# Optimization experiments

Hardware: AMD Instinct MI355X
Metric: run time of the kernel (lower is better)

## Reference

```python
import jax, jax.numpy as jnp
import numpy as np

B, T, D, H = 64, 512, 1024, 2048


def setup_inputs() -> dict:
    key = jax.random.key(0)
    ks = jax.random.split(key, 7)
    s_ih = 1.0 / np.sqrt(H)
    return {
        "x": jax.random.normal(ks[0], (B, T, D), dtype=jnp.float32),
        "W_ih": jax.random.normal(ks[1], (4 * H, D), dtype=jnp.float32) * s_ih,
        "W_hh": jax.random.normal(ks[2], (4 * H, H), dtype=jnp.float32) * s_ih,
        "b_ih": jax.random.normal(ks[3], (4 * H,), dtype=jnp.float32) * s_ih,
        "b_hh": jax.random.normal(ks[4], (4 * H,), dtype=jnp.float32) * s_ih,
        "W_head": jax.random.normal(ks[5], (D, H), dtype=jnp.float32) * (1.0 / np.sqrt(H)),
        "b_head": jax.random.normal(ks[6], (D,), dtype=jnp.float32) * 0.01,
    }


def reference(x, W_ih, W_hh, b_ih, b_hh, W_head, b_head):
    Bn, Tn, Dn = x.shape
    Hn = W_hh.shape[1]
    # precompute input projections for all timesteps: [T, B, 4H]
    x_proj = jnp.einsum('btd,gd->tbg', x, W_ih) + (b_ih + b_hh)

    def step(carry, xp_t):
        h, c = carry
        gates = xp_t + h @ W_hh.T  # [B, 4H]
        i, f, g, o = jnp.split(gates, 4, axis=-1)  # PyTorch gate order: i,f,g,o
        i = jax.nn.sigmoid(i)
        f = jax.nn.sigmoid(f)
        g = jnp.tanh(g)
        o = jax.nn.sigmoid(o)
        c = f * c + i * g
        h = o * jnp.tanh(c)
        return (h, c), None

    h0 = jnp.zeros((Bn, Hn), dtype=x.dtype)
    c0 = jnp.zeros((Bn, Hn), dtype=x.dtype)
    (h, c), _ = jax.lax.scan(step, (h0, c0), x_proj)
    return h @ W_head.T + b_head  # [B, D]
```

## Files before the change

kernel.cpp:

```cpp
#include <hip/hip_runtime.h>
#include <hip/hip_bf16.h>
#include <cstdint>
#include <cstddef>

#define BB 64
#define TT 512
#define DD 1024
#define HH 2048
#define GG 8192

typedef unsigned short u16;
typedef __attribute__((ext_vector_type(8))) short bf16x8;
typedef __attribute__((ext_vector_type(4))) float f32x4;

__device__ __forceinline__ u16 f2bf(float f) {
  union { float f; uint32_t u; } v; v.f = f;
  uint32_t r = v.u + 0x7FFFu + ((v.u >> 16) & 1u);
  return (u16)(r >> 16);
}
__device__ __forceinline__ float bf2f(u16 h) {
  union { uint32_t u; float f; } v; v.u = ((uint32_t)h) << 16; return v.f;
}

__device__ __forceinline__ bf16x8 cvt8(const float* __restrict__ p) {
  float4 a = *(const float4*)p;
  float4 b = *(const float4*)(p + 4);
  bf16x8 r;
  r[0] = (short)f2bf(a.x); r[1] = (short)f2bf(a.y);
  r[2] = (short)f2bf(a.z); r[3] = (short)f2bf(a.w);
  r[4] = (short)f2bf(b.x); r[5] = (short)f2bf(b.y);
  r[6] = (short)f2bf(b.z); r[7] = (short)f2bf(b.w);
  return r;
}

__device__ __forceinline__ bf16x8 cohload16(const u16* p) {
  bf16x8 v;
  asm volatile("global_load_dwordx4 %0, %1, off sc0 sc1" : "=v"(v) : "v"(p));
  return v;
}
__device__ __forceinline__ void cohstore16(u16* p, bf16x8 v) {
  asm volatile("global_store_dwordx4 %0, %1, off sc0 sc1" :: "v"(p), "v"(v) : "memory");
}

__global__ void conv_wih_kernel(const float* __restrict__ W, u16* __restrict__ Wb) {
  size_t idx = (size_t)blockIdx.x * blockDim.x + threadIdx.x;
  if (idx >= (size_t)GG * DD / 8) return;
  *(bf16x8*)(Wb + idx * 8) = cvt8(W + idx * 8);
}

__global__ void conv_xT_kernel(const float* __restrict__ x, u16* __restrict__ xbT) {
  size_t idx = (size_t)blockIdx.x * blockDim.x + threadIdx.x;
  if (idx >= (size_t)BB * TT * DD / 8) return;
  const int col8 = (int)(idx & 127);
  const int row = (int)(idx >> 7);
  const int b = row >> 9, t = row & 511;
  bf16x8 v = cvt8(x + (size_t)row * DD + col8 * 8);
  *(bf16x8*)(xbT + ((size_t)t * BB + b) * DD + col8 * 8) = v;
}

template<int XMODE>
__global__ __launch_bounds__(512, 1)
void lstm_persistent(const float* __restrict__ x, const u16* __restrict__ xbT,
                     const u16* __restrict__ wihb, const float* __restrict__ W_hh,
                     const float* __restrict__ b_ih, const float* __restrict__ b_hh,
                     u16* __restrict__ h0, u16* __restrict__ h1,
                     int* __restrict__ arrv, int* __restrict__ gof) {
  __shared__ u16 Wlds[64 * 2 * 64 * 8];
  __shared__ float red[4 * 2 * 64 * 4];
  __shared__ float gst[64 * 36];
  __shared__ u16 hsh[512];

  const int tid = threadIdx.x;
  const int wave = tid >> 6, lane = tid & 63;
  const int m = wave & 3, khalf = wave >> 2;
  const int c = lane & 15, g = lane >> 4;
  const int wg = blockIdx.x, j0 = wg * 8;

  {
    const int r = tid >> 4;
    const int gr = (r < 8) ? (j0 + r) : (r < 16) ? (HH + j0 + r - 8)
                 : (r < 24) ? (2 * HH + j0 + r - 16) : (3 * HH + j0 + r - 24);
    const int which = r >> 4, cc = r & 15;
    const float* src = W_hh + (size_t)gr * HH;
    const int k0 = (tid & 15) * 128;
    #pragma unroll
    for (int k8 = 0; k8 < 16; ++k8) {
      const int k = k0 + k8 * 8;
      bf16x8 v = cvt8(src + k);
      const int ent = ((k >> 5) * 2 + which) * 64 + ((k >> 3) & 3) * 16 + cc;
      *(bf16x8*)(Wlds + (size_t)ent * 8) = v;
    }
  }

  const int tb = tid >> 3, tj = tid & 7;
  const int jg = j0 + tj;
  const float bia = b_ih[jg] + b_hh[jg];
  const float bfa = b_ih[HH + jg] + b_hh[HH + jg];
  const float bga = b_ih[2 * HH + jg] + b_hh[2 * HH + jg];
  const float boa = b_ih[3 * HH + jg] + b_hh[3 * HH + jg];
  float cst = 0.f;

  const int arow = m * 16 + c;
  const int r0 = (c < 8) ? (j0 + c) : (HH + j0 + c - 8);
  const int r1 = (c < 8) ? (2 * HH + j0 + c) : (3 * HH + j0 + c - 8);

  __syncthreads();

  for (int t = 0; t < TT; ++t) {
    const u16* hs = (t & 1) ? h1 : h0;
    u16* hd = (t & 1) ? h0 : h1;
    f32x4 acc0 = {0.f, 0.f, 0.f, 0.f};
    f32x4 acc1 = {0.f, 0.f, 0.f, 0.f};

    #pragma unroll 4
    for (int i = 0; i < 16; ++i) {
      const int k = khalf * 512 + i * 32 + g * 8;
      bf16x8 a;
      if constexpr (XMODE == 1) a = *(const bf16x8*)(xbT + ((size_t)t * BB + arow) * DD + k);
      else                      a = cvt8(x + ((size_t)arow * TT + t) * DD + k);
      bf16x8 b0 = *(const bf16x8*)(wihb + (size_t)r0 * DD + k);
      bf16x8 b1 = *(const bf16x8*)(wihb + (size_t)r1 * DD + k);
      acc0 = __builtin_amdgcn_mfma_f32_16x16x32_bf16(a, b0, acc0, 0, 0, 0);
      acc1 = __builtin_amdgcn_mfma_f32_16x16x32_bf16(a, b1, acc1, 0, 0, 0);
    }

    if (t > 0) {
      if (wg == 0) {
        if (tid < 256) {
          int iters = 0;
          while (__hip_atomic_load(arrv + tid * 16, __ATOMIC_RELAXED, __HIP_MEMORY_SCOPE_AGENT) < t) {
            __builtin_amdgcn_s_sleep(1);
            if (++iters > (1 << 17)) break;
          }
        }
        __syncthreads();
        if (tid < 256)
          __hip_atomic_store(gof + tid * 16, t, __ATOMIC_RELAXED, __HIP_MEMORY_SCOPE_AGENT);
      } else {
        if (tid == 0) {
          int iters = 0;
          while (__hip_atomic_load(gof + wg * 16, __ATOMIC_RELAXED, __HIP_MEMORY_SCOPE_AGENT) < t) {
            __builtin_amdgcn_s_sleep(1);
            if (++iters > (1 << 17)) break;
          }
        }
      }
    }
    __syncthreads();

    {
      bf16x8 hf[32];
      const u16* hrow = hs + (size_t)arow * HH + g * 8;
      #pragma unroll
      for (int i = 0; i < 32; ++i)
        hf[i] = cohload16(hrow + (size_t)(khalf * 32 + i) * 32);

      #pragma unroll
      for (int grp = 0; grp < 4; ++grp) {
        if (grp == 0)      asm volatile("s_waitcnt vmcnt(24)" ::: "memory");
        else if (grp == 1) asm volatile("s_waitcnt vmcnt(16)" ::: "memory");
        else if (grp == 2) asm volatile("s_waitcnt vmcnt(8)"  ::: "memory");
        else               asm volatile("s_waitcnt vmcnt(0)"  ::: "memory");
        __builtin_amdgcn_sched_barrier(0);
        #pragma unroll
        for (int i2 = 0; i2 < 8; ++i2) {
          const int i = grp * 8 + i2;
          const int kb = khalf * 32 + i;
          bf16x8 b0 = *(const bf16x8*)(Wlds + (size_t)((kb * 2 + 0) * 64 + lane) * 8);
          bf16x8 b1 = *(const bf16x8*)(Wlds + (size_t)((kb * 2 + 1) * 64 + lane) * 8);
          acc0 = __builtin_amdgcn_mfma_f32_16x16x32_bf16(hf[i], b0, acc0, 0, 0, 0);
          acc1 = __builtin_amdgcn_mfma_f32_16x16x32_bf16(hf[i], b1, acc1, 0, 0, 0);
        }
      }
    }

    if (khalf == 1) {
      #pragma unroll
      for (int q = 0; q < 4; ++q) {
        red[((m * 2 + 0) * 64 + lane) * 4 + q] = acc0[q];
        red[((m * 2 + 1) * 64 + lane) * 4 + q] = acc1[q];
      }
    }
    __syncthreads();
    if (khalf == 0) {
      #pragma unroll
      for (int q = 0; q < 4; ++q) {
        const float s0 = acc0[q] + red[((m * 2 + 0) * 64 + lane) * 4 + q];
        const float s1 = acc1[q] + red[((m * 2 + 1) * 64 + lane) * 4 + q];
        const int b = m * 16 + g * 4 + q;
        gst[b * 36 + c] = s0;
        gst[b * 36 + 16 + c] = s1;
      }
    }
    __syncthreads();

    {
      const float ip = gst[tb * 36 + tj]      + bia;
      const float fp = gst[tb * 36 + 8 + tj]  + bfa;
      const float gp = gst[tb * 36 + 16 + tj] + bga;
      const float op = gst[tb * 36 + 24 + tj] + boa;
      const float ig = 1.f / (1.f + expf(-ip));
      const float fg = 1.f / (1.f + expf(-fp));
      const float gv = tanhf(gp);
      const float og = 1.f / (1.f + expf(-op));
      cst = fg * cst + ig * gv;
      hsh[tb * 8 + tj] = f2bf(og * tanhf(cst));
    }
    __syncthreads();

    if (tid < 64) {
      bf16x8 v = *(const bf16x8*)(hsh + tid * 8);
      cohstore16(hd + (size_t)tid * HH + j0, v);
      asm volatile("s_waitcnt vmcnt(0)" ::: "memory");
    }
    __syncthreads();
    if (tid == 0)
      __hip_atomic_store(arrv + wg * 16, t + 1, __ATOMIC_RELAXED, __HIP_MEMORY_SCOPE_AGENT);
  }
}

__global__ __launch_bounds__(512)
void lstm_step_kernel(const float* __restrict__ x,
                      const float* __restrict__ W_ih, const float* __restrict__ W_hh,
                      const float* __restrict__ b_ih, const float* __restrict__ b_hh,
                      const u16* __restrict__ h_src, u16* __restrict__ h_dst,
                      float* __restrict__ cbuf, int t) {
  const int tid = threadIdx.x;
  const int wave = tid >> 6, lane = tid & 63;
  const int m = wave & 3, khalf = wave >> 2;
  const int j0 = blockIdx.x * 8;
  const int c = lane & 15;
  const int arow = m * 16 + c;
  const int koff = (lane >> 4) * 8;
  const int r0 = (c < 8) ? (j0 + c) : (HH + j0 + c - 8);
  const int r1 = (c < 8) ? (2 * HH + j0 + c) : (3 * HH + j0 + c - 8);

  f32x4 acc0 = {0.f, 0.f, 0.f, 0.f};
  f32x4 acc1 = {0.f, 0.f, 0.f, 0.f};

  if (khalf == 0) {
    const size_t xrow = ((size_t)arow * TT + t) * DD;
    #pragma unroll 4
    for (int kb = 0; kb < 32; ++kb) {
      const int k = kb * 32 + koff;
      bf16x8 a = cvt8(x + xrow + k);
      bf16x8 b0 = cvt8(W_ih + (size_t)r0 * DD + k);
      bf16x8 b1 = cvt8(W_ih + (size_t)r1 * DD + k);
      acc0 = __builtin_amdgcn_mfma_f32_16x16x32_bf16(a, b0, acc0, 0, 0, 0);
      acc1 = __builtin_amdgcn_mfma_f32_16x16x32_bf16(a, b1, acc1, 0, 0, 0);
    }
    #pragma unroll 4
    for (int kb = 0; kb < 16; ++kb) {
      const int kh = kb * 32 + koff;
      bf16x8 a = *(const bf16x8*)(h_src + (size_t)arow * HH + kh);
      bf16x8 b0 = cvt8(W_hh + (size_t)r0 * HH + kh);
      bf16x8 b1 = cvt8(W_hh + (size_t)r1 * HH + kh);
      acc0 = __builtin_amdgcn_mfma_f32_16x16x32_bf16(a, b0, acc0, 0, 0, 0);
      acc1 = __builtin_amdgcn_mfma_f32_16x16x32_bf16(a, b1, acc1, 0, 0, 0);
    }
  } else {
    #pragma unroll 4
    for (int kb = 0; kb < 48; ++kb) {
      const int kh = 512 + kb * 32 + koff;
      bf16x8 a = *(const bf16x8*)(h_src + (size_t)arow * HH + kh);
      bf16x8 b0 = cvt8(W_hh + (size_t)r0 * HH + kh);
      bf16x8 b1 = cvt8(W_hh + (size_t)r1 * HH + kh);
      acc0 = __builtin_amdgcn_mfma_f32_16x16x32_bf16(a, b0, acc0, 0, 0, 0);
      acc1 = __builtin_amdgcn_mfma_f32_16x16x32_bf16(a, b1, acc1, 0, 0, 0);
    }
  }

  __shared__ float red[4][2][64][4];
  if (khalf == 1) {
    #pragma unroll
    for (int q = 0; q < 4; ++q) { red[m][0][lane][q] = acc0[q]; red[m][1][lane][q] = acc1[q]; }
  }
  __syncthreads();
  if (khalf == 1) return;
  #pragma unroll
  for (int q = 0; q < 4; ++q) { acc0[q] += red[m][0][lane][q]; acc1[q] += red[m][1][lane][q]; }

  const float bias0 = b_ih[r0] + b_hh[r0];
  const float bias1 = b_ih[r1] + b_hh[r1];
  #pragma unroll
  for (int q = 0; q < 4; ++q) { acc0[q] += bias0; acc1[q] += bias1; }

  float fpre[4], opre[4];
  #pragma unroll
  for (int q = 0; q < 4; ++q) {
    fpre[q] = __shfl_xor(acc0[q], 8);
    opre[q] = __shfl_xor(acc1[q], 8);
  }

  if (c < 8) {
    const int j = j0 + c;
    #pragma unroll
    for (int q = 0; q < 4; ++q) {
      const int b = m * 16 + (lane >> 4) * 4 + q;
      const float ig = 1.f / (1.f + expf(-acc0[q]));
      const float fg = 1.f / (1.f + expf(-fpre[q]));
      const float gg = tanhf(acc1[q]);
      const float og = 1.f / (1.f + expf(-opre[q]));
      const float cold = cbuf[(size_t)b * HH + j];
      const float cn = fg * cold + ig * gg;
      cbuf[(size_t)b * HH + j] = cn;
      h_dst[(size_t)b * HH + j] = f2bf(og * tanhf(cn));
    }
  }
}

__global__ __launch_bounds__(256)
void head_kernel(const u16* __restrict__ hfin, const float* __restrict__ W_head,
                 const float* __restrict__ b_head, float* __restrict__ out) {
  const int tid = threadIdx.x, wave = tid >> 6, lane = tid & 63;
  const int m = wave;
  const int c = lane & 15;
  const int koff = (lane >> 4) * 8;
  const int d = blockIdx.x * 16 + c;
  const int arow = m * 16 + c;
  f32x4 acc = {0.f, 0.f, 0.f, 0.f};
  #pragma unroll 4
  for (int kb = 0; kb < 64; ++kb) {
    const int k = kb * 32 + koff;
    bf16x8 a = *(const bf16x8*)(hfin + (size_t)arow * HH + k);
    bf16x8 b = cvt8(W_head + (size_t)d * HH + k);
    acc = __builtin_amdgcn_mfma_f32_16x16x32_bf16(a, b, acc, 0, 0, 0);
  }
  const float bh = b_head[d];
  #pragma unroll
  for (int q = 0; q < 4; ++q) {
    const int b = m * 16 + (lane >> 4) * 4 + q;
    out[(size_t)b * DD + d] = acc[q] + bh;
  }
}

extern "C" void kernel_launch(void* const* d_in, const int* in_sizes, int n_in,
                              void* d_out, int out_size, void* d_ws, size_t ws_size,
                              hipStream_t stream) {
  const float* x      = (const float*)d_in[0];
  const float* W_ih   = (const float*)d_in[1];
  const float* W_hh   = (const float*)d_in[2];
  const float* b_ih   = (const float*)d_in[3];
  const float* b_hh   = (const float*)d_in[4];
  const float* W_head = (const float*)d_in[5];
  const float* b_head = (const float*)d_in[6];
  float* out = (float*)d_out;

  char* ws = (char*)d_ws;
  u16*  h0    = (u16*)(ws + 0);
  u16*  h1    = (u16*)(ws + 256 * 1024);
  int*  arrv  = (int*)(ws + 512 * 1024);
  int*  gof   = (int*)(ws + 544 * 1024);
  float* cbuf = (float*)(ws + 512 * 1024);
  u16*  wihb  = (u16*)(ws + (1ull << 20));
  u16*  xbT   = (u16*)(ws + (17ull << 20));

  const size_t NEED1 = (81ull << 20);
  const size_t NEED0 = (17ull << 20);

  hipMemsetAsync(ws, 0, 1u << 20, stream);

  if (ws_size >= NEED0) {
    {
      const int n8 = (int)((size_t)GG * DD / 8);
      conv_wih_kernel<<<(n8 + 255) / 256, 256, 0, stream>>>(W_ih, wihb);
    }
    if (ws_size >= NEED1) {
      const int n8 = (int)((size_t)BB * TT * DD / 8);
      conv_xT_kernel<<<(n8 + 255) / 256, 256, 0, stream>>>(x, xbT);
      lstm_persistent<1><<<256, 512, 0, stream>>>(x, xbT, wihb, W_hh, b_ih, b_hh, h0, h1, arrv, gof);
    } else {
      lstm_persistent<0><<<256, 512, 0, stream>>>(x, xbT, wihb, W_hh, b_ih, b_hh, h0, h1, arrv, gof);
    }
  } else {
    for (int t = 0; t < TT; ++t) {
      u16* hs = (t & 1) ? h1 : h0;
      u16* hd = (t & 1) ? h0 : h1;
      lstm_step_kernel<<<256, 512, 0, stream>>>(x, W_ih, W_hh, b_ih, b_hh, hs, hd, cbuf, t);
    }
  }

  head_kernel<<<64, 256, 0, stream>>>(h0, W_head, b_head, out);
}
```

Measured before the change: 10.46 ms.

## Stage hidden state per XCD into L2 before recurrent matmul loads

Each workgroup finds its XCD and takes a rank within it. At every timestep the 32 workgroups on that XCD copy the full hidden state from the coherent buffer into a per-XCD staging buffer and meet at a per-XCD counter barrier. The recurrent matmul then reads h with L2-cacheable loads instead of loads that bypass the cache to memory. This is meant to cut the latency and memory traffic of 256 workgroups all reading h uncached. The cost is an extra copy, an extra barrier per step, and the assumption that exactly 32 workgroups land on each XCD.

```diff
diff --git a/kernel.cpp b/kernel.cpp
--- a/kernel.cpp
+++ b/kernel.cpp
@@ -41,6 +41,16 @@
 __device__ __forceinline__ void cohstore16(u16* p, bf16x8 v) {
   asm volatile("global_store_dwordx4 %0, %1, off sc0 sc1" :: "v"(p), "v"(v) : "memory");
 }
+__device__ __forceinline__ bf16x8 l2load16(const u16* p) {
+  bf16x8 v;
+  asm volatile("global_load_dwordx4 %0, %1, off sc0" : "=v"(v) : "v"(p));
+  return v;
+}
+__device__ __forceinline__ int get_xcd() {
+  int x;
+  asm("s_getreg_b32 %0, hwreg(20, 0, 32)" : "=s"(x));
+  return x & 7;
+}
 
 __global__ void conv_wih_kernel(const float* __restrict__ W, u16* __restrict__ Wb) {
   size_t idx = (size_t)blockIdx.x * blockDim.x + threadIdx.x;
@@ -64,17 +74,27 @@
                      const u16* __restrict__ wihb, const float* __restrict__ W_hh,
                      const float* __restrict__ b_ih, const float* __restrict__ b_hh,
                      u16* __restrict__ h0, u16* __restrict__ h1,
-                     int* __restrict__ arrv, int* __restrict__ gof) {
+                     int* __restrict__ arrv, int* __restrict__ gof,
+                     int* __restrict__ ximp, int* __restrict__ xcdcnt,
+                     u16* __restrict__ staged) {
   __shared__ u16 Wlds[64 * 2 * 64 * 8];
   __shared__ float red[4 * 2 * 64 * 4];
   __shared__ float gst[64 * 36];
   __shared__ u16 hsh[512];
+  __shared__ int sxcd, srank;
 
   const int tid = threadIdx.x;
   const int wave = tid >> 6, lane = tid & 63;
   const int m = wave & 3, khalf = wave >> 2;
   const int c = lane & 15, g = lane >> 4;
   const int wg = blockIdx.x, j0 = wg * 8;
+
+  if (tid == 0) {
+    const int xd = get_xcd();
+    sxcd = xd;
+    srank = __hip_atomic_fetch_add(xcdcnt + xd * 16, 1, __ATOMIC_RELAXED,
+                                   __HIP_MEMORY_SCOPE_AGENT);
+  }
 
   {
     const int r = tid >> 4;
@@ -105,10 +125,13 @@
   const int r1 = (c < 8) ? (2 * HH + j0 + c) : (3 * HH + j0 + c - 8);
 
   __syncthreads();
+  const int xcd = sxcd, rank = srank & 31;
+  int* xctr = ximp + xcd * 16;
 
   for (int t = 0; t < TT; ++t) {
     const u16* hs = (t & 1) ? h1 : h0;
     u16* hd = (t & 1) ? h0 : h1;
+    u16* stg = staged + ((size_t)xcd * 2 + (t & 1)) * ((size_t)BB * HH);
     f32x4 acc0 = {0.f, 0.f, 0.f, 0.f};
     f32x4 acc1 = {0.f, 0.f, 0.f, 0.f};
 
@@ -149,11 +172,30 @@
     __syncthreads();
 
     {
+      const int row = rank * 2 + (tid >> 8);
+      const int col = (tid & 255) * 8;
+      bf16x8 v = cohload16(hs + (size_t)row * HH + col);
+      asm volatile("s_waitcnt vmcnt(0)" ::: "memory");
+      cohstore16(stg + (size_t)row * HH + col, v);
+      asm volatile("s_waitcnt vmcnt(0)" ::: "memory");
+    }
+    __syncthreads();
+    if (tid == 0) {
+      __hip_atomic_fetch_add(xctr, 1, __ATOMIC_RELAXED, __HIP_MEMORY_SCOPE_AGENT);
+      int iters = 0;
+      while (__hip_atomic_load(xctr, __ATOMIC_RELAXED, __HIP_MEMORY_SCOPE_AGENT) < 32 * (t + 1)) {
+        __builtin_amdgcn_s_sleep(1);
+        if (++iters > (1 << 17)) break;
+      }
+    }
+    __syncthreads();
+
+    {
       bf16x8 hf[32];
-      const u16* hrow = hs + (size_t)arow * HH + g * 8;
+      const u16* hrow = stg + (size_t)arow * HH + g * 8;
       #pragma unroll
       for (int i = 0; i < 32; ++i)
-        hf[i] = cohload16(hrow + (size_t)(khalf * 32 + i) * 32);
+        hf[i] = l2load16(hrow + (size_t)(khalf * 32 + i) * 32);
 
       #pragma unroll
       for (int grp = 0; grp < 4; ++grp) {
@@ -347,16 +389,19 @@
   float* out = (float*)d_out;
 
   char* ws = (char*)d_ws;
-  u16*  h0    = (u16*)(ws + 0);
-  u16*  h1    = (u16*)(ws + 256 * 1024);
-  int*  arrv  = (int*)(ws + 512 * 1024);
-  int*  gof   = (int*)(ws + 544 * 1024);
-  float* cbuf = (float*)(ws + 512 * 1024);
-  u16*  wihb  = (u16*)(ws + (1ull << 20));
-  u16*  xbT   = (u16*)(ws + (17ull << 20));
-
-  const size_t NEED1 = (81ull << 20);
-  const size_t NEED0 = (17ull << 20);
+  u16*  h0     = (u16*)(ws + 0);
+  u16*  h1     = (u16*)(ws + 256 * 1024);
+  int*  arrv   = (int*)(ws + 512 * 1024);
+  int*  gof    = (int*)(ws + 544 * 1024);
+  int*  ximp   = (int*)(ws + 576 * 1024);
+  int*  xcdcnt = (int*)(ws + 608 * 1024);
+  float* cbuf  = (float*)(ws + 512 * 1024);
+  u16*  staged = (u16*)(ws + (1ull << 20));
+  u16*  wihb   = (u16*)(ws + (5ull << 20));
+  u16*  xbT    = (u16*)(ws + (21ull << 20));
+
+  const size_t NEED1 = (85ull << 20);
+  const size_t NEED0 = (21ull << 20);
 
   hipMemsetAsync(ws, 0, 1u << 20, stream);
 
@@ -368,9 +413,11 @@
     if (ws_size >= NEED1) {
       const int n8 = (int)((size_t)BB * TT * DD / 8);
       conv_xT_kernel<<<(n8 + 255) / 256, 256, 0, stream>>>(x, xbT);
-      lstm_persistent<1><<<256, 512, 0, stream>>>(x, xbT, wihb, W_hh, b_ih, b_hh, h0, h1, arrv, gof);
+      lstm_persistent<1><<<256, 512, 0, stream>>>(x, xbT, wihb, W_hh, b_ih, b_hh,
+                                                  h0, h1, arrv, gof, ximp, xcdcnt, staged);
     } else {
-      lstm_persistent<0><<<256, 512, 0, stream>>>(x, xbT, wihb, W_hh, b_ih, b_hh, h0, h1, arrv, gof);
+      lstm_persistent<0><<<256, 512, 0, stream>>>(x, xbT, wihb, W_hh, b_ih, b_hh,
+                                                  h0, h1, arrv, gof, ximp, xcdcnt, staged);
     }
   } else {
     for (int t = 0; t < TT; ++t) {
```

Result: slower. 12.42 ms (+18.7%).

## Replace centralized grid barrier with grouped atomic counters polled per wave

Applied to the files above, without the earlier changes.

Drops the two-level barrier, in which block 0 gathered 256 arrival flags and then released every block. Each block now does a fetch_add on one of 8 group counters, and every wave polls the 4 counters covering its K half of h, starting at a rotated position. This takes the block-0 round trip and a __syncthreads out of the serial per-step critical path. hsh is double-buffered so the trailing __syncthreads can go, at the cost of more atomic contention on shared counters.

```diff
diff --git a/kernel.cpp b/kernel.cpp
--- a/kernel.cpp
+++ b/kernel.cpp
@@ -42,6 +42,15 @@
   asm volatile("global_store_dwordx4 %0, %1, off sc0 sc1" :: "v"(p), "v"(v) : "memory");
 }
 
+__device__ __forceinline__ void wait_ctr(const int* ctr, int target) {
+  int iters = 0;
+  while (__hip_atomic_load(ctr, __ATOMIC_RELAXED, __HIP_MEMORY_SCOPE_AGENT) < target) {
+    __builtin_amdgcn_s_sleep(1);
+    if (++iters > (1 << 17)) break;
+  }
+  __builtin_amdgcn_sched_barrier(0);
+}
+
 __global__ void conv_wih_kernel(const float* __restrict__ W, u16* __restrict__ Wb) {
   size_t idx = (size_t)blockIdx.x * blockDim.x + threadIdx.x;
   if (idx >= (size_t)GG * DD / 8) return;
@@ -64,17 +73,18 @@
                      const u16* __restrict__ wihb, const float* __restrict__ W_hh,
                      const float* __restrict__ b_ih, const float* __restrict__ b_hh,
                      u16* __restrict__ h0, u16* __restrict__ h1,
-                     int* __restrict__ arrv, int* __restrict__ gof) {
+                     int* __restrict__ gctr) {
   __shared__ u16 Wlds[64 * 2 * 64 * 8];
   __shared__ float red[4 * 2 * 64 * 4];
   __shared__ float gst[64 * 36];
-  __shared__ u16 hsh[512];
+  __shared__ u16 hsh[2][512];
 
   const int tid = threadIdx.x;
   const int wave = tid >> 6, lane = tid & 63;
   const int m = wave & 3, khalf = wave >> 2;
-  const int c = lane & 15, g = lane >> 4;
+  const int c = lane & 15, lofs = lane >> 4;
   const int wg = blockIdx.x, j0 = wg * 8;
+  const int mygrp = wg >> 5;
 
   {
     const int r = tid >> 4;
@@ -104,6 +114,12 @@
   const int r0 = (c < 8) ? (j0 + c) : (HH + j0 + c - 8);
   const int r1 = (c < 8) ? (2 * HH + j0 + c) : (3 * HH + j0 + c - 8);
 
+  const int rot = wg & 3;
+  const int pg0 = khalf * 4 + ((0 + rot) & 3);
+  const int pg1 = khalf * 4 + ((1 + rot) & 3);
+  const int pg2 = khalf * 4 + ((2 + rot) & 3);
+  const int pg3 = khalf * 4 + ((3 + rot) & 3);
+
   __syncthreads();
 
   for (int t = 0; t < TT; ++t) {
@@ -114,7 +130,7 @@
 
     #pragma unroll 4
     for (int i = 0; i < 16; ++i) {
-      const int k = khalf * 512 + i * 32 + g * 8;
+      const int k = khalf * 512 + i * 32 + lofs * 8;
       bf16x8 a;
       if constexpr (XMODE == 1) a = *(const bf16x8*)(xbT + ((size_t)t * BB + arow) * DD + k);
       else                      a = cvt8(x + ((size_t)arow * TT + t) * DD + k);
@@ -125,32 +141,16 @@
     }
 
     if (t > 0) {
-      if (wg == 0) {
-        if (tid < 256) {
-          int iters = 0;
-          while (__hip_atomic_load(arrv + tid * 16, __ATOMIC_RELAXED, __HIP_MEMORY_SCOPE_AGENT) < t) {
-            __builtin_amdgcn_s_sleep(1);
-            if (++iters > (1 << 17)) break;
-          }
-        }
-        __syncthreads();
-        if (tid < 256)
-          __hip_atomic_store(gof + tid * 16, t, __ATOMIC_RELAXED, __HIP_MEMORY_SCOPE_AGENT);
-      } else {
-        if (tid == 0) {
-          int iters = 0;
-          while (__hip_atomic_load(gof + wg * 16, __ATOMIC_RELAXED, __HIP_MEMORY_SCOPE_AGENT) < t) {
-            __builtin_amdgcn_s_sleep(1);
-            if (++iters > (1 << 17)) break;
-          }
-        }
-      }
-    }
-    __syncthreads();
+      const int tgt = 32 * t;
+      wait_ctr(gctr + pg0 * 16, tgt);
+      wait_ctr(gctr + pg1 * 16, tgt);
+      wait_ctr(gctr + pg2 * 16, tgt);
+      wait_ctr(gctr + pg3 * 16, tgt);
+    }
 
     {
       bf16x8 hf[32];
-      const u16* hrow = hs + (size_t)arow * HH + g * 8;
+      const u16* hrow = hs + (size_t)arow * HH + lofs * 8;
       #pragma unroll
       for (int i = 0; i < 32; ++i)
         hf[i] = cohload16(hrow + (size_t)(khalf * 32 + i) * 32);
@@ -187,7 +187,7 @@
       for (int q = 0; q < 4; ++q) {
         const float s0 = acc0[q] + red[((m * 2 + 0) * 64 + lane) * 4 + q];
         const float s1 = acc1[q] + red[((m * 2 + 1) * 64 + lane) * 4 + q];
-        const int b = m * 16 + g * 4 + q;
+        const int b = m * 16 + lofs * 4 + q;
         gst[b * 36 + c] = s0;
         gst[b * 36 + 16 + c] = s1;
       }
@@ -204,18 +204,18 @@
       const float gv = tanhf(gp);
       const float og = 1.f / (1.f + expf(-op));
       cst = fg * cst + ig * gv;
-      hsh[tb * 8 + tj] = f2bf(og * tanhf(cst));
+      hsh[t & 1][tb * 8 + tj] = f2bf(og * tanhf(cst));
     }
     __syncthreads();
 
     if (tid < 64) {
-      bf16x8 v = *(const bf16x8*)(hsh + tid * 8);
+      bf16x8 v = *(const bf16x8*)(&hsh[t & 1][tid * 8]);
       cohstore16(hd + (size_t)tid * HH + j0, v);
       asm volatile("s_waitcnt vmcnt(0)" ::: "memory");
     }
-    __syncthreads();
     if (tid == 0)
-      __hip_atomic_store(arrv + wg * 16, t + 1, __ATOMIC_RELAXED, __HIP_MEMORY_SCOPE_AGENT);
+      __hip_atomic_fetch_add(gctr + mygrp * 16, 1, __ATOMIC_RELAXED,
+                             __HIP_MEMORY_SCOPE_AGENT);
   }
 }
 
@@ -349,8 +349,7 @@
   char* ws = (char*)d_ws;
   u16*  h0    = (u16*)(ws + 0);
   u16*  h1    = (u16*)(ws + 256 * 1024);
-  int*  arrv  = (int*)(ws + 512 * 1024);
-  int*  gof   = (int*)(ws + 544 * 1024);
+  int*  gctr  = (int*)(ws + 512 * 1024);
   float* cbuf = (float*)(ws + 512 * 1024);
   u16*  wihb  = (u16*)(ws + (1ull << 20));
   u16*  xbT   = (u16*)(ws + (17ull << 20));
@@ -368,9 +367,11 @@
     if (ws_size >= NEED1) {
       const int n8 = (int)((size_t)BB * TT * DD / 8);
       conv_xT_kernel<<<(n8 + 255) / 256, 256, 0, stream>>>(x, xbT);
-      lstm_persistent<1><<<256, 512, 0, stream>>>(x, xbT, wihb, W_hh, b_ih, b_hh, h0, h1, arrv, gof);
+      lstm_persistent<1><<<256, 512, 0, stream>>>(x, xbT, wihb, W_hh, b_ih, b_hh,
+                                                  h0, h1, gctr);
     } else {
-      lstm_persistent<0><<<256, 512, 0, stream>>>(x, xbT, wihb, W_hh, b_ih, b_hh, h0, h1, arrv, gof);
+      lstm_persistent<0><<<256, 512, 0, stream>>>(x, xbT, wihb, W_hh, b_ih, b_hh,
+                                                  h0, h1, gctr);
     }
   } else {
     for (int t = 0; t < TT; ++t) {
```

Measured after the change: 10.42 ms (median of 2 runs). Within noise of the previous version (-0.4%).

## Partition recurrent matmul by XCD with register-resident W_hh and split-K exchange

Applied to the files above, without the earlier changes.

Restructures the persistent LSTM kernel so each workgroup reads its XCD id at runtime and takes a rank within that XCD. Each workgroup keeps a slice of W_hh in registers, computes split-K partial gate products over its XCD's 256-wide hidden slice, and exchanges bf16 partials through a global buffer. Hidden state is synchronised per XCD with local flags instead of a global barrier through workgroup 0. The aim is to keep h traffic inside each XCD's L2 and remove the global barrier. In exchange it adds a second all-to-all exchange per step, rounds partials to bf16, and assumes exactly 32 workgroups land on each of the 8 XCDs.

```diff
diff --git a/kernel.cpp b/kernel.cpp
--- a/kernel.cpp
+++ b/kernel.cpp
@@ -41,6 +41,11 @@
 __device__ __forceinline__ void cohstore16(u16* p, bf16x8 v) {
   asm volatile("global_store_dwordx4 %0, %1, off sc0 sc1" :: "v"(p), "v"(v) : "memory");
 }
+__device__ __forceinline__ int get_xcd() {
+  int x;
+  asm("s_getreg_b32 %0, hwreg(20, 0, 32)" : "=s"(x));
+  return x & 7;
+}
 
 __global__ void conv_wih_kernel(const float* __restrict__ W, u16* __restrict__ Wb) {
   size_t idx = (size_t)blockIdx.x * blockDim.x + threadIdx.x;
@@ -63,159 +68,214 @@
 void lstm_persistent(const float* __restrict__ x, const u16* __restrict__ xbT,
                      const u16* __restrict__ wihb, const float* __restrict__ W_hh,
                      const float* __restrict__ b_ih, const float* __restrict__ b_hh,
-                     u16* __restrict__ h0, u16* __restrict__ h1,
-                     int* __restrict__ arrv, int* __restrict__ gof) {
-  __shared__ u16 Wlds[64 * 2 * 64 * 8];
-  __shared__ float red[4 * 2 * 64 * 4];
-  __shared__ float gst[64 * 36];
-  __shared__ u16 hsh[512];
+                     u16* __restrict__ Lh, int* __restrict__ pflag,
+                     int* __restrict__ lhflag, int* __restrict__ xcdcnt,
+                     u16* __restrict__ Pbuf) {
+  __shared__ u16 pstage[64 * 264];
+  __shared__ u16 pr[8 * 4 * 64 * 8];
+  __shared__ float xstage[32 * 66];
+  __shared__ char occ_pad[32768];
+  __shared__ int sxcd, srank;
 
   const int tid = threadIdx.x;
   const int wave = tid >> 6, lane = tid & 63;
-  const int m = wave & 3, khalf = wave >> 2;
-  const int c = lane & 15, g = lane >> 4;
-  const int wg = blockIdx.x, j0 = wg * 8;
-
+  const int c16 = lane & 15, lofs = lane >> 4;
+
+  if (tid == 0) {
+    const int xd = get_xcd();
+    sxcd = xd;
+    srank = __hip_atomic_fetch_add(xcdcnt + xd * 16, 1, __ATOMIC_RELAXED,
+                                   __HIP_MEMORY_SCOPE_AGENT);
+  }
+  __syncthreads();
+  const int xcd = sxcd, rank = srank & 31;
+  if (xcd > 8) occ_pad[0] = 1;
+
+  bf16x8 Wreg[2][8];
   {
-    const int r = tid >> 4;
-    const int gr = (r < 8) ? (j0 + r) : (r < 16) ? (HH + j0 + r - 8)
-                 : (r < 24) ? (2 * HH + j0 + r - 16) : (3 * HH + j0 + r - 24);
-    const int which = r >> 4, cc = r & 15;
-    const float* src = W_hh + (size_t)gr * HH;
-    const int k0 = (tid & 15) * 128;
+    const int growb = 256 * rank + wave * 32;
     #pragma unroll
-    for (int k8 = 0; k8 < 16; ++k8) {
-      const int k = k0 + k8 * 8;
-      bf16x8 v = cvt8(src + k);
-      const int ent = ((k >> 5) * 2 + which) * 64 + ((k >> 3) & 3) * 16 + cc;
-      *(bf16x8*)(Wlds + (size_t)ent * 8) = v;
-    }
-  }
-
-  const int tb = tid >> 3, tj = tid & 7;
-  const int jg = j0 + tj;
-  const float bia = b_ih[jg] + b_hh[jg];
-  const float bfa = b_ih[HH + jg] + b_hh[HH + jg];
-  const float bga = b_ih[2 * HH + jg] + b_hh[2 * HH + jg];
-  const float boa = b_ih[3 * HH + jg] + b_hh[3 * HH + jg];
+    for (int nt2 = 0; nt2 < 2; ++nt2)
+      #pragma unroll
+      for (int kb = 0; kb < 8; ++kb)
+        Wreg[nt2][kb] = cvt8(W_hh + (size_t)(growb + nt2 * 16 + c16) * HH
+                                   + 256 * xcd + kb * 32 + lofs * 8);
+  }
+
+  const int ng = wave & 1, mt4 = wave >> 1;
+  const int xrow = ng * 16 + c16;
+  const int xg = (xrow >> 3) * HH + 256 * xcd + 8 * rank + (xrow & 7);
+  const u16* wihrow = wihb + (size_t)xg * DD;
+
+  const int eb = tid >> 3, ejl = tid & 7;
+  const int jg = 256 * xcd + 8 * rank + ejl;
+  const float bi0 = b_ih[jg] + b_hh[jg];
+  const float bi1 = b_ih[HH + jg] + b_hh[HH + jg];
+  const float bi2 = b_ih[2 * HH + jg] + b_hh[2 * HH + jg];
+  const float bi3 = b_ih[3 * HH + jg] + b_hh[3 * HH + jg];
   float cst = 0.f;
 
+  const int xdst = rank & 7, mprod = rank >> 3;
+  int* myPflag = pflag + (xcd * 32 + rank) * 16;
+  int* myLhflag = lhflag + (xcd * 32 + rank) * 16;
+
+  for (int t = 0; t < TT; ++t) {
+    const int pp = t & 1, pread = pp ^ 1, pwrite = pp;
+
+    {
+      f32x4 xacc = {0.f, 0.f, 0.f, 0.f};
+      const size_t aoff = XMODE ? ((size_t)(t * BB + mt4 * 16 + c16) * DD)
+                                : (((size_t)(mt4 * 16 + c16) * TT + t) * DD);
+      #pragma unroll 8
+      for (int kb = 0; kb < 32; ++kb) {
+        const int k = kb * 32 + lofs * 8;
+        bf16x8 a;
+        if constexpr (XMODE == 1) a = *(const bf16x8*)(xbT + aoff + k);
+        else                      a = cvt8(x + aoff + k);
+        bf16x8 bf = *(const bf16x8*)(wihrow + k);
+        xacc = __builtin_amdgcn_mfma_f32_16x16x32_bf16(a, bf, xacc, 0, 0, 0);
+      }
+      #pragma unroll
+      for (int q = 0; q < 4; ++q)
+        xstage[xrow * 66 + mt4 * 16 + lofs * 4 + q] = xacc[q];
+    }
+
+    if (t > 0 && wave == 0) {
+      const int* fl = lhflag + (xcd * 32 + (lane & 31)) * 16;
+      int iters = 0;
+      while (true) {
+        asm volatile("buffer_inv sc0" ::: "memory");
+        int v;
+        asm volatile("global_load_dword %0, %1, off\n\ts_waitcnt vmcnt(0)"
+                     : "=v"(v) : "v"(fl) : "memory");
+        if (__all(v >= t)) break;
+        __builtin_amdgcn_s_sleep(2);
+        if (++iters > (1 << 17)) break;
+      }
+      asm volatile("buffer_inv sc0" ::: "memory");
+    }
+    __syncthreads();
+
+    {
+      f32x4 pacc[4][2] = {};
+      const u16* lhb = Lh + ((size_t)(xcd * 2 + pread) * 64) * 256;
+      #pragma unroll
+      for (int kb = 0; kb < 8; ++kb) {
+        bf16x8 af[4];
+        #pragma unroll
+        for (int mt = 0; mt < 4; ++mt)
+          af[mt] = *(const bf16x8*)(lhb + (size_t)(mt * 16 + c16) * 256 + kb * 32 + lofs * 8);
+        #pragma unroll
+        for (int mt = 0; mt < 4; ++mt) {
+          pacc[mt][0] = __builtin_amdgcn_mfma_f32_16x16x32_bf16(af[mt], Wreg[0][kb], pacc[mt][0], 0, 0, 0);
+          pacc[mt][1] = __builtin_amdgcn_mfma_f32_16x16x32_bf16(af[mt], Wreg[1][kb], pacc[mt][1], 0, 0, 0);
+        }
+      }
+      #pragma unroll
+      for (int mt = 0; mt < 4; ++mt)
+        #pragma unroll
+        for (int nt2 = 0; nt2 < 2; ++nt2)
+          #pragma unroll
+          for (int q = 0; q < 4; ++q)
+            pstage[(mt * 16 + lofs * 4 + q) * 264 + wave * 32 + nt2 * 16 + c16]
+                = f2bf(pacc[mt][nt2][q]);
+    }
+    __syncthreads();
+
+    {
+      const int jc = tid >> 4, b0 = (tid & 15) * 4;
+      u16* dst = Pbuf + ((size_t)(xdst * 2 + pp) << 19)
+                      + (size_t)((jc * 8 + xcd) * 4 + mprod) * 512;
+      #pragma unroll
+      for (int i = 0; i < 4; ++i) {
+        const int b = b0 + i;
+        bf16x8 v = *(const bf16x8*)(pstage + b * 264 + jc * 8);
+        cohstore16(dst + b * 8, v);
+      }
+      asm volatile("s_waitcnt vmcnt(0)" ::: "memory");
+    }
+    __syncthreads();
+    if (tid == 0)
+      __hip_atomic_store(myPflag, t + 1, __ATOMIC_RELAXED, __HIP_MEMORY_SCOPE_AGENT);
+
+    if (wave == 0) {
+      const int l2 = lane & 31;
+      const int* sfl = pflag + ((l2 >> 2) * 32 + (l2 & 3) * 8 + xcd) * 16;
+      int iters = 0;
+      while (true) {
+        int v = __hip_atomic_load(sfl, __ATOMIC_RELAXED, __HIP_MEMORY_SCOPE_AGENT);
+        if (__all(v >= t + 1)) break;
+        __builtin_amdgcn_s_sleep(2);
+        if (++iters > (1 << 17)) break;
+      }
+    }
+    __syncthreads();
+    {
+      const u16* src = Pbuf + ((size_t)(xcd * 2 + pp) << 19) + (size_t)rank * 16384;
+      bf16x8 v0 = cohload16(src + (0 * 512 + tid) * 8);
+      bf16x8 v1 = cohload16(src + (1 * 512 + tid) * 8);
+      bf16x8 v2 = cohload16(src + (2 * 512 + tid) * 8);
+      bf16x8 v3 = cohload16(src + (3 * 512 + tid) * 8);
+      asm volatile("s_waitcnt vmcnt(0)" ::: "memory");
+      __builtin_amdgcn_sched_barrier(0);
+      *(bf16x8*)(pr + (0 * 512 + tid) * 8) = v0;
+      *(bf16x8*)(pr + (1 * 512 + tid) * 8) = v1;
+      *(bf16x8*)(pr + (2 * 512 + tid) * 8) = v2;
+      *(bf16x8*)(pr + (3 * 512 + tid) * 8) = v3;
+    }
+    __syncthreads();
+
+    {
+      float g4[4];
+      #pragma unroll
+      for (int m = 0; m < 4; ++m) {
+        float s = 0.f;
+        #pragma unroll
+        for (int y = 0; y < 8; ++y)
+          s += bf2f(pr[((y * 4 + m) * 64 + eb) * 8 + ejl]);
+        g4[m] = s + xstage[(m * 8 + ejl) * 66 + eb];
+      }
+      const float ig = 1.f / (1.f + expf(-(g4[0] + bi0)));
+      const float fg = 1.f / (1.f + expf(-(g4[1] + bi1)));
+      const float gv = tanhf(g4[2] + bi2);
+      const float og = 1.f / (1.f + expf(-(g4[3] + bi3)));
+      cst = fg * cst + ig * gv;
+      const uint32_t hv = (uint32_t)f2bf(og * tanhf(cst));
+      u16* hp = Lh + ((size_t)(xcd * 2 + pwrite) * 64 + eb) * 256 + 8 * rank + ejl;
+      asm volatile("global_store_short %0, %1, off" :: "v"(hp), "v"(hv) : "memory");
+      asm volatile("s_waitcnt vmcnt(0)" ::: "memory");
+    }
+    __syncthreads();
+    if (tid == 0) {
+      const int tv = t + 1;
+      asm volatile("global_store_dword %0, %1, off" :: "v"(myLhflag), "v"(tv) : "memory");
+    }
+  }
+}
+
+__global__ __launch_bounds__(256)
+void head_lh_kernel(const u16* __restrict__ Lh, const float* __restrict__ W_head,
+                    const float* __restrict__ b_head, float* __restrict__ out) {
+  const int tid = threadIdx.x, wave = tid >> 6, lane = tid & 63;
+  const int m = wave;
+  const int c = lane & 15;
+  const int koff = (lane >> 4) * 8;
+  const int d = blockIdx.x * 16 + c;
   const int arow = m * 16 + c;
-  const int r0 = (c < 8) ? (j0 + c) : (HH + j0 + c - 8);
-  const int r1 = (c < 8) ? (2 * HH + j0 + c) : (3 * HH + j0 + c - 8);
-
-  __syncthreads();
-
-  for (int t = 0; t < TT; ++t) {
-    const u16* hs = (t & 1) ? h1 : h0;
-    u16* hd = (t & 1) ? h0 : h1;
-    f32x4 acc0 = {0.f, 0.f, 0.f, 0.f};
-    f32x4 acc1 = {0.f, 0.f, 0.f, 0.f};
-
-    #pragma unroll 4
-    for (int i = 0; i < 16; ++i) {
-      const int k = khalf * 512 + i * 32 + g * 8;
-      bf16x8 a;
-      if constexpr (XMODE == 1) a = *(const bf16x8*)(xbT + ((size_t)t * BB + arow) * DD + k);
-      else                      a = cvt8(x + ((size_t)arow * TT + t) * DD + k);
-      bf16x8 b0 = *(const bf16x8*)(wihb + (size_t)r0 * DD + k);
-      bf16x8 b1 = *(const bf16x8*)(wihb + (size_t)r1 * DD + k);
-      acc0 = __builtin_amdgcn_mfma_f32_16x16x32_bf16(a, b0, acc0, 0, 0, 0);
-      acc1 = __builtin_amdgcn_mfma_f32_16x16x32_bf16(a, b1, acc1, 0, 0, 0);
-    }
-
-    if (t > 0) {
-      if (wg == 0) {
-        if (tid < 256) {
-          int iters = 0;
-          while (__hip_atomic_load(arrv + tid * 16, __ATOMIC_RELAXED, __HIP_MEMORY_SCOPE_AGENT) < t) {
-            __builtin_amdgcn_s_sleep(1);
-            if (++iters > (1 << 17)) break;
-          }
-        }
-        __syncthreads();
-        if (tid < 256)
-          __hip_atomic_store(gof + tid * 16, t, __ATOMIC_RELAXED, __HIP_MEMORY_SCOPE_AGENT);
-      } else {
-        if (tid == 0) {
-          int iters = 0;
-          while (__hip_atomic_load(gof + wg * 16, __ATOMIC_RELAXED, __HIP_MEMORY_SCOPE_AGENT) < t) {
-            __builtin_amdgcn_s_sleep(1);
-            if (++iters > (1 << 17)) break;
-          }
-        }
-      }
-    }
-    __syncthreads();
-
-    {
-      bf16x8 hf[32];
-      const u16* hrow = hs + (size_t)arow * HH + g * 8;
-      #pragma unroll
-      for (int i = 0; i < 32; ++i)
-        hf[i] = cohload16(hrow + (size_t)(khalf * 32 + i) * 32);
-
-      #pragma unroll
-      for (int grp = 0; grp < 4; ++grp) {
-        if (grp == 0)      asm volatile("s_waitcnt vmcnt(24)" ::: "memory");
-        else if (grp == 1) asm volatile("s_waitcnt vmcnt(16)" ::: "memory");
-        else if (grp == 2) asm volatile("s_waitcnt vmcnt(8)"  ::: "memory");
-        else               asm volatile("s_waitcnt vmcnt(0)"  ::: "memory");
-        __builtin_amdgcn_sched_barrier(0);
-        #pragma unroll
-        for (int i2 = 0; i2 < 8; ++i2) {
-          const int i = grp * 8 + i2;
-          const int kb = khalf * 32 + i;
-          bf16x8 b0 = *(const bf16x8*)(Wlds + (size_t)((kb * 2 + 0) * 64 + lane) * 8);
-          bf16x8 b1 = *(const bf16x8*)(Wlds + (size_t)((kb * 2 + 1) * 64 + lane) * 8);
-          acc0 = __builtin_amdgcn_mfma_f32_16x16x32_bf16(hf[i], b0, acc0, 0, 0, 0);
-          acc1 = __builtin_amdgcn_mfma_f32_16x16x32_bf16(hf[i], b1, acc1, 0, 0, 0);
-        }
-      }
-    }
-
-    if (khalf == 1) {
-      #pragma unroll
-      for (int q = 0; q < 4; ++q) {
-        red[((m * 2 + 0) * 64 + lane) * 4 + q] = acc0[q];
-        red[((m * 2 + 1) * 64 + lane) * 4 + q] = acc1[q];
-      }
-    }
-    __syncthreads();
-    if (khalf == 0) {
-      #pragma unroll
-      for (int q = 0; q < 4; ++q) {
-        const float s0 = acc0[q] + red[((m * 2 + 0) * 64 + lane) * 4 + q];
-        const float s1 = acc1[q] + red[((m * 2 + 1) * 64 + lane) * 4 + q];
-        const int b = m * 16 + g * 4 + q;
-        gst[b * 36 + c] = s0;
-        gst[b * 36 + 16 + c] = s1;
-      }
-    }
-    __syncthreads();
-
-    {
-      const float ip = gst[tb * 36 + tj]      + bia;
-      const float fp = gst[tb * 36 + 8 + tj]  + bfa;
-      const float gp = gst[tb * 36 + 16 + tj] + bga;
-      const float op = gst[tb * 36 + 24 + tj] + boa;
-      const float ig = 1.f / (1.f + expf(-ip));
-      const float fg = 1.f / (1.f + expf(-fp));
-      const float gv = tanhf(gp);
-      const float og = 1.f / (1.f + expf(-op));
-      cst = fg * cst + ig * gv;
-      hsh[tb * 8 + tj] = f2bf(og * tanhf(cst));
-    }
-    __syncthreads();
-
-    if (tid < 64) {
-      bf16x8 v = *(const bf16x8*)(hsh + tid * 8);
-      cohstore16(hd + (size_t)tid * HH + j0, v);
-      asm volatile("s_waitcnt vmcnt(0)" ::: "memory");
-    }
-    __syncthreads();
-    if (tid == 0)
-      __hip_atomic_store(arrv + wg * 16, t + 1, __ATOMIC_RELAXED, __HIP_MEMORY_SCOPE_AGENT);
+  f32x4 acc = {0.f, 0.f, 0.f, 0.f};
+  #pragma unroll 4
+  for (int kb = 0; kb < 64; ++kb) {
+    const int k = kb * 32 + koff;
+    const int xk = k >> 8, jloc = k & 255;
+    bf16x8 a = *(const bf16x8*)(Lh + ((size_t)(xk * 2 + 1) * 64 + arow) * 256 + jloc);
+    bf16x8 b = cvt8(W_head + (size_t)d * HH + k);
+    acc = __builtin_amdgcn_mfma_f32_16x16x32_bf16(a, b, acc, 0, 0, 0);
+  }
+  const float bh = b_head[d];
+  #pragma unroll
+  for (int q = 0; q < 4; ++q) {
+    const int b = m * 16 + (lane >> 4) * 4 + q;
+    out[(size_t)b * DD + d] = acc[q] + bh;
   }
 }
 
@@ -347,16 +407,20 @@
   float* out = (float*)d_out;
 
   char* ws = (char*)d_ws;
+  u16*  Lh     = (u16*)(ws + 0);
+  int*  pflag  = (int*)(ws + 512 * 1024);
+  int*  lhflag = (int*)(ws + 528 * 1024);
+  int*  xcdcnt = (int*)(ws + 544 * 1024);
+  u16*  Pbuf   = (u16*)(ws + (1ull << 20));
+  u16*  wihb   = (u16*)(ws + (17ull << 20));
+  u16*  xbT    = (u16*)(ws + (33ull << 20));
+
   u16*  h0    = (u16*)(ws + 0);
   u16*  h1    = (u16*)(ws + 256 * 1024);
-  int*  arrv  = (int*)(ws + 512 * 1024);
-  int*  gof   = (int*)(ws + 544 * 1024);
   float* cbuf = (float*)(ws + 512 * 1024);
-  u16*  wihb  = (u16*)(ws + (1ull << 20));
-  u16*  xbT   = (u16*)(ws + (17ull << 20));
-
-  const size_t NEED1 = (81ull << 20);
-  const size_t NEED0 = (17ull << 20);
+
+  const size_t NEED1 = (97ull << 20);
+  const size_t NEED0 = (33ull << 20);
 
   hipMemsetAsync(ws, 0, 1u << 20, stream);
 
@@ -368,17 +432,19 @@
     if (ws_size >= NEED1) {
       const int n8 = (int)((size_t)BB * TT * DD / 8);
       conv_xT_kernel<<<(n8 + 255) / 256, 256, 0, stream>>>(x, xbT);
-      lstm_persistent<1><<<256, 512, 0, stream>>>(x, xbT, wihb, W_hh, b_ih, b_hh, h0, h1, arrv, gof);
+      lstm_persistent<1><<<256, 512, 0, stream>>>(x, xbT, wihb, W_hh, b_ih, b_hh,
+                                                  Lh, pflag, lhflag, xcdcnt, Pbuf);
     } else {
-      lstm_persistent<0><<<256, 512, 0, stream>>>(x, xbT, wihb, W_hh, b_ih, b_hh, h0, h1, arrv, gof);
-    }
+      lstm_persistent<0><<<256, 512, 0, stream>>>(x, xbT, wihb, W_hh, b_ih, b_hh,
+                                                  Lh, pflag, lhflag, xcdcnt, Pbuf);
+    }
+    head_lh_kernel<<<64, 256, 0, stream>>>(Lh, W_head, b_head, out);
   } else {
     for (int t = 0; t < TT; ++t) {
       u16* hs = (t & 1) ? h1 : h0;
       u16* hd = (t & 1) ? h0 : h1;
       lstm_step_kernel<<<256, 512, 0, stream>>>(x, W_ih, W_hh, b_ih, b_hh, hs, hd, cbuf, t);
     }
-  }
-
-  head_kernel<<<64, 256, 0, stream>>>(h0, W_head, b_head, out);
-}
+    head_kernel<<<64, 256, 0, stream>>>(h0, W_head, b_head, out);
+  }
+}
```

Measured after the change: 16.34 ms. 1.56x slower.
